# Kernel optimization log

Measured on AMD Instinct MI355X. Metric: run time of the kernel, lower is better.

## Reference

```python
import jax, jax.numpy as jnp
import numpy as np

B, N, DIN, DOUT = 8192, 4, 1024, 256

def setup_inputs() -> dict:
    key = jax.random.key(0)
    k1, k2, k3, k4 = jax.random.split(key, 4)
    adj = jax.random.uniform(k1, (N, N), dtype=jnp.float32)
    features = jax.random.normal(k2, (B, N, DIN), dtype=jnp.float32)
    # nn.Linear(input_size, output_size): weight [DOUT, DIN], bias [DOUT]
    bound = 1.0 / np.sqrt(DIN)
    W = jax.random.uniform(k3, (DOUT, DIN), dtype=jnp.float32, minval=-bound, maxval=bound)
    b = jax.random.uniform(k4, (DOUT,), dtype=jnp.float32, minval=-bound, maxval=bound)
    return {"adj": adj, "features": features, "W": W, "b": b}

def reference(adj, features, W, b):
    # Batched equivalent of: for i in B: linear(adj @ features[i]) -> [B, 4, DOUT]
    h = jnp.einsum("nm,bmf->bnf", adj, features)  # [B, N, DIN]
    return jnp.einsum("bnf,of->bno", h, W) + b    # [B, N, DOUT]
```

## Files before the change

kernel.cpp:

```cpp
#include <hip/hip_runtime.h>


#define DIN 1024
#define DOUT 256
#define BM 64
#define BK 64
#define KI 16
#define LDB 72
#define WS_PER_KB (DOUT * LDB)
#define A_HALFS (BM * LDB)
#define B_HALFS (DOUT * LDB)

typedef __bf16 bf16x8 __attribute__((ext_vector_type(8)));
typedef float f32x4 __attribute__((ext_vector_type(4)));
typedef unsigned short u16x8 __attribute__((ext_vector_type(8)));

__device__ __forceinline__ unsigned short f2bf(float f) {
  union { float f; unsigned int u; } v;
  v.f = f;
  unsigned int u = v.u;
  u += 0x7fffu + ((u >> 16) & 1u);
  return (unsigned short)(u >> 16);
}

__device__ __forceinline__ void glds16(const unsigned short* g, unsigned short* l) {
  __builtin_amdgcn_global_load_lds(
      (const __attribute__((address_space(1))) void*)g,
      (__attribute__((address_space(3))) void*)l, 16, 0, 0);
}

__global__ __launch_bounds__(256) void wprep_kernel(
    const float* __restrict__ W, unsigned short* __restrict__ ws) {
  const int t = blockIdx.x * 256 + threadIdx.x;
  const int col = t >> 7;
  const int k8 = t & 127;
  const int kb = k8 >> 3;
  const int kc = (k8 & 7) * 8;
  const f32x4* src = (const f32x4*)(W + (size_t)col * DIN + k8 * 8);
  f32x4 a = src[0], b = src[1];
  u16x8 pk;
#pragma unroll
  for (int m = 0; m < 4; ++m) {
    pk[m] = f2bf(a[m]);
    pk[4 + m] = f2bf(b[m]);
  }
  unsigned short* dst = ws + (size_t)kb * WS_PER_KB + col * LDB + kc;
  *(u16x8*)dst = pk;
  if ((k8 & 7) == 7) {
    u16x8 z = {0, 0, 0, 0, 0, 0, 0, 0};
    *(u16x8*)(ws + (size_t)kb * WS_PER_KB + col * LDB + 64) = z;
  }
}

__global__ __launch_bounds__(256, 2) void gconv_kernel(
    const float* __restrict__ adj, const float* __restrict__ feat,
    const unsigned short* __restrict__ wbf, const float* __restrict__ bias,
    float* __restrict__ out) {
  __shared__ __align__(16) unsigned short sB[B_HALFS];
  __shared__ __align__(16) unsigned short sA[A_HALFS];
  __shared__ float sbias[DOUT];

  const int tid = threadIdx.x;
  const int bM = blockIdx.x * BM;

  sbias[tid] = bias[tid];

  const int row0 = tid >> 3;
  const int kc0 = (tid & 7) * 8;
  const int row1 = (tid + 256) >> 3;
  const float* aptr0 = feat + (size_t)(bM + row0) * DIN + kc0;
  const float* aptr1 = feat + (size_t)(bM + row1) * DIN + kc0;
  unsigned short* sAw0 = sA + row0 * LDB + kc0;
  unsigned short* sAw1 = sA + row1 * LDB + kc0;

  const int lane = tid & 63;
  const int wid = tid >> 6;
  const int wc = wid * 64;
  const int rl = lane & 15;
  const int q = lane >> 4;

  f32x4 acc[4][4];
#pragma unroll
  for (int i = 0; i < 4; ++i)
#pragma unroll
    for (int j = 0; j < 4; ++j) acc[i][j] = f32x4{0.f, 0.f, 0.f, 0.f};

  f32x4 pa0 = *(const f32x4*)aptr0;
  f32x4 pa1 = *(const f32x4*)(aptr0 + 4);
  f32x4 pa2 = *(const f32x4*)aptr1;
  f32x4 pa3 = *(const f32x4*)(aptr1 + 4);
  aptr0 += BK;
  aptr1 += BK;

  for (int kb = 0; kb < KI; ++kb) {
    const unsigned short* bs = wbf + (size_t)kb * WS_PER_KB;
#pragma unroll
    for (int r = 0; r < 9; ++r) {
      const int idx = r * 256 + tid;
      glds16(bs + idx * 8, sB + idx * 8);
    }

    u16x8 pk0, pk1;
#pragma unroll
    for (int m = 0; m < 4; ++m) {
      pk0[m] = f2bf(pa0[m]);
      pk0[4 + m] = f2bf(pa1[m]);
      pk1[m] = f2bf(pa2[m]);
      pk1[4 + m] = f2bf(pa3[m]);
    }
    if (kb + 1 < KI) {
      pa0 = *(const f32x4*)aptr0;
      pa1 = *(const f32x4*)(aptr0 + 4);
      pa2 = *(const f32x4*)aptr1;
      pa3 = *(const f32x4*)(aptr1 + 4);
      aptr0 += BK;
      aptr1 += BK;
    }
    *(u16x8*)sAw0 = pk0;
    *(u16x8*)sAw1 = pk1;
    __syncthreads();

#pragma unroll
    for (int ks = 0; ks < 2; ++ks) {
      const int ko = ks * 32 + q * 8;
      bf16x8 af[4], bfr[4];
#pragma unroll
      for (int i = 0; i < 4; ++i)
        af[i] = *(const bf16x8*)(sA + (i * 16 + rl) * LDB + ko);
#pragma unroll
      for (int j = 0; j < 4; ++j)
        bfr[j] = *(const bf16x8*)(sB + (wc + j * 16 + rl) * LDB + ko);
#pragma unroll
      for (int i = 0; i < 4; ++i)
#pragma unroll
        for (int j = 0; j < 4; ++j)
          acc[i][j] = __builtin_amdgcn_mfma_f32_16x16x32_bf16(af[i], bfr[j],
                                                              acc[i][j], 0, 0, 0);
    }
    __syncthreads();
  }

  float am[16];
#pragma unroll
  for (int i = 0; i < 16; ++i) am[i] = adj[i];

  float bv[4];
#pragma unroll
  for (int j = 0; j < 4; ++j) bv[j] = sbias[wc + j * 16 + rl];

#pragma unroll
  for (int i = 0; i < 4; ++i) {
    const size_t rowbase = (size_t)(bM + i * 16 + q * 4);
#pragma unroll
    for (int j = 0; j < 4; ++j) {
      const int col = wc + j * 16 + rl;
      float* op = out + rowbase * DOUT + col;
      f32x4 g = acc[i][j];
#pragma unroll
      for (int n = 0; n < 4; ++n) {
        op[(size_t)n * DOUT] = am[n * 4 + 0] * g[0] + am[n * 4 + 1] * g[1] +
                               am[n * 4 + 2] * g[2] + am[n * 4 + 3] * g[3] +
                               bv[j];
      }
    }
  }
}

extern "C" void kernel_launch(void* const* d_in, const int* in_sizes, int n_in,
                              void* d_out, int out_size, void* d_ws,
                              size_t ws_size, hipStream_t stream) {
  const float* adj = (const float*)d_in[0];
  const float* feat = (const float*)d_in[1];
  const float* W = (const float*)d_in[2];
  const float* bias = (const float*)d_in[3];
  float* out = (float*)d_out;
  unsigned short* ws = (unsigned short*)d_ws;

  wprep_kernel<<<128, 256, 0, stream>>>(W, ws);
  gconv_kernel<<<8192 * 4 / BM, 256, 0, stream>>>(adj, feat, ws, bias, out);
}
```

Before: 219.7 us.

## Load bf16 weights directly into registers and double-buffer A tile in LDS

```diff
diff --git a/kernel.cpp b/kernel.cpp
--- a/kernel.cpp
+++ b/kernel.cpp
@@ -4,12 +4,9 @@
 #define DIN 1024
 #define DOUT 256
 #define BM 64
-#define BK 64
 #define KI 16
 #define LDB 72
-#define WS_PER_KB (DOUT * LDB)
 #define A_HALFS (BM * LDB)
-#define B_HALFS (DOUT * LDB)
 
 typedef __bf16 bf16x8 __attribute__((ext_vector_type(8)));
 typedef float f32x4 __attribute__((ext_vector_type(4)));
@@ -23,20 +20,10 @@
   return (unsigned short)(u >> 16);
 }
 
-__device__ __forceinline__ void glds16(const unsigned short* g, unsigned short* l) {
-  __builtin_amdgcn_global_load_lds(
-      (const __attribute__((address_space(1))) void*)g,
-      (__attribute__((address_space(3))) void*)l, 16, 0, 0);
-}
-
 __global__ __launch_bounds__(256) void wprep_kernel(
     const float* __restrict__ W, unsigned short* __restrict__ ws) {
   const int t = blockIdx.x * 256 + threadIdx.x;
-  const int col = t >> 7;
-  const int k8 = t & 127;
-  const int kb = k8 >> 3;
-  const int kc = (k8 & 7) * 8;
-  const f32x4* src = (const f32x4*)(W + (size_t)col * DIN + k8 * 8);
+  const f32x4* src = (const f32x4*)(W + (size_t)t * 8);
   f32x4 a = src[0], b = src[1];
   u16x8 pk;
 #pragma unroll
@@ -44,40 +31,33 @@
     pk[m] = f2bf(a[m]);
     pk[4 + m] = f2bf(b[m]);
   }
-  unsigned short* dst = ws + (size_t)kb * WS_PER_KB + col * LDB + kc;
-  *(u16x8*)dst = pk;
-  if ((k8 & 7) == 7) {
-    u16x8 z = {0, 0, 0, 0, 0, 0, 0, 0};
-    *(u16x8*)(ws + (size_t)kb * WS_PER_KB + col * LDB + 64) = z;
-  }
+  *(u16x8*)(ws + (size_t)t * 8) = pk;
 }
 
-__global__ __launch_bounds__(256, 2) void gconv_kernel(
+__global__ __launch_bounds__(256, 3) void gconv_kernel(
     const float* __restrict__ adj, const float* __restrict__ feat,
     const unsigned short* __restrict__ wbf, const float* __restrict__ bias,
     float* __restrict__ out) {
-  __shared__ __align__(16) unsigned short sB[B_HALFS];
-  __shared__ __align__(16) unsigned short sA[A_HALFS];
-  __shared__ float sbias[DOUT];
+  __shared__ __align__(16) unsigned short sA[2][A_HALFS];
 
   const int tid = threadIdx.x;
   const int bM = blockIdx.x * BM;
 
-  sbias[tid] = bias[tid];
-
   const int row0 = tid >> 3;
   const int kc0 = (tid & 7) * 8;
-  const int row1 = (tid + 256) >> 3;
   const float* aptr0 = feat + (size_t)(bM + row0) * DIN + kc0;
-  const float* aptr1 = feat + (size_t)(bM + row1) * DIN + kc0;
-  unsigned short* sAw0 = sA + row0 * LDB + kc0;
-  unsigned short* sAw1 = sA + row1 * LDB + kc0;
+  const float* aptr1 = aptr0 + (size_t)32 * DIN;
+  unsigned short* sw0 = &sA[0][row0 * LDB + kc0];
+  unsigned short* sw1 = &sA[1][row0 * LDB + kc0];
 
   const int lane = tid & 63;
   const int wid = tid >> 6;
   const int wc = wid * 64;
   const int rl = lane & 15;
   const int q = lane >> 4;
+  const int q8 = q * 8;
+
+  const unsigned short* bp0 = wbf + (size_t)(wc + rl) * DIN + q8;
 
   f32x4 acc[4][4];
 #pragma unroll
@@ -89,17 +69,7 @@
   f32x4 pa1 = *(const f32x4*)(aptr0 + 4);
   f32x4 pa2 = *(const f32x4*)aptr1;
   f32x4 pa3 = *(const f32x4*)(aptr1 + 4);
-  aptr0 += BK;
-  aptr1 += BK;
-
-  for (int kb = 0; kb < KI; ++kb) {
-    const unsigned short* bs = wbf + (size_t)kb * WS_PER_KB;
-#pragma unroll
-    for (int r = 0; r < 9; ++r) {
-      const int idx = r * 256 + tid;
-      glds16(bs + idx * 8, sB + idx * 8);
-    }
-
+  {
     u16x8 pk0, pk1;
 #pragma unroll
     for (int m = 0; m < 4; ++m) {
@@ -108,36 +78,65 @@
       pk1[m] = f2bf(pa2[m]);
       pk1[4 + m] = f2bf(pa3[m]);
     }
-    if (kb + 1 < KI) {
-      pa0 = *(const f32x4*)aptr0;
-      pa1 = *(const f32x4*)(aptr0 + 4);
-      pa2 = *(const f32x4*)aptr1;
-      pa3 = *(const f32x4*)(aptr1 + 4);
-      aptr0 += BK;
-      aptr1 += BK;
-    }
-    *(u16x8*)sAw0 = pk0;
-    *(u16x8*)sAw1 = pk1;
-    __syncthreads();
+    *(u16x8*)sw0 = pk0;
+    *(u16x8*)(sw0 + 32 * LDB) = pk1;
+  }
+  pa0 = *(const f32x4*)(aptr0 + 64);
+  pa1 = *(const f32x4*)(aptr0 + 68);
+  pa2 = *(const f32x4*)(aptr1 + 64);
+  pa3 = *(const f32x4*)(aptr1 + 68);
 
+  for (int kb = 0; kb < KI; ++kb) {
+    bf16x8 bfr[2][4];
+#pragma unroll
+    for (int ks = 0; ks < 2; ++ks)
+#pragma unroll
+      for (int j = 0; j < 4; ++j)
+        bfr[ks][j] =
+            *(const bf16x8*)(bp0 + (size_t)j * 16 * DIN + kb * 64 + ks * 32);
+
+    __builtin_amdgcn_sched_barrier(0);
+    asm volatile("s_waitcnt lgkmcnt(0)" ::: "memory");
+    __builtin_amdgcn_s_barrier();
+    __builtin_amdgcn_sched_barrier(0);
+
+    const unsigned short* sa = (kb & 1) ? &sA[1][0] : &sA[0][0];
 #pragma unroll
     for (int ks = 0; ks < 2; ++ks) {
-      const int ko = ks * 32 + q * 8;
-      bf16x8 af[4], bfr[4];
+      const int ko = ks * 32 + q8;
+      bf16x8 af[4];
 #pragma unroll
       for (int i = 0; i < 4; ++i)
-        af[i] = *(const bf16x8*)(sA + (i * 16 + rl) * LDB + ko);
-#pragma unroll
-      for (int j = 0; j < 4; ++j)
-        bfr[j] = *(const bf16x8*)(sB + (wc + j * 16 + rl) * LDB + ko);
+        af[i] = *(const bf16x8*)(sa + (i * 16 + rl) * LDB + ko);
 #pragma unroll
       for (int i = 0; i < 4; ++i)
 #pragma unroll
         for (int j = 0; j < 4; ++j)
-          acc[i][j] = __builtin_amdgcn_mfma_f32_16x16x32_bf16(af[i], bfr[j],
-                                                              acc[i][j], 0, 0, 0);
+          acc[i][j] = __builtin_amdgcn_mfma_f32_16x16x32_bf16(
+              af[i], bfr[ks][j], acc[i][j], 0, 0, 0);
     }
-    __syncthreads();
+
+    if (kb + 1 < KI) {
+      u16x8 pk0, pk1;
+#pragma unroll
+      for (int m = 0; m < 4; ++m) {
+        pk0[m] = f2bf(pa0[m]);
+        pk0[4 + m] = f2bf(pa1[m]);
+        pk1[m] = f2bf(pa2[m]);
+        pk1[4 + m] = f2bf(pa3[m]);
+      }
+      unsigned short* sw = ((kb + 1) & 1) ? sw1 : sw0;
+      *(u16x8*)sw = pk0;
+      *(u16x8*)(sw + 32 * LDB) = pk1;
+      if (kb + 2 < KI) {
+        const float* a0 = aptr0 + (size_t)(kb + 2) * 64;
+        const float* a1 = aptr1 + (size_t)(kb + 2) * 64;
+        pa0 = *(const f32x4*)a0;
+        pa1 = *(const f32x4*)(a0 + 4);
+        pa2 = *(const f32x4*)a1;
+        pa3 = *(const f32x4*)(a1 + 4);
+      }
+    }
   }
 
   float am[16];
@@ -146,7 +145,7 @@
 
   float bv[4];
 #pragma unroll
-  for (int j = 0; j < 4; ++j) bv[j] = sbias[wc + j * 16 + rl];
+  for (int j = 0; j < 4; ++j) bv[j] = bias[wc + j * 16 + rl];
 
 #pragma unroll
   for (int i = 0; i < 4; ++i) {
```

Result: no change. 222.4 us (+1.2%).
